# Kernel optimization log

Measured on AMD Instinct MI355X. Metric: run time of the kernel, lower is better.

Reference implementation:

```python
import jax, jax.numpy as jnp
from jax import lax
import numpy as np

DECAY = 0.9
THRESH = 1.0


def setup_inputs() -> dict:
    key = jax.random.key(0)
    k1, k2, k3 = jax.random.split(key, 3)
    B, T, I, H, O = 64, 256, 1024, 2048, 1024
    x = jax.random.normal(k1, (B, T, I), dtype=jnp.float32)
    W1 = jax.random.normal(k2, (I, H), dtype=jnp.float32) * (1.0 / np.sqrt(I))
    b1 = jnp.zeros((H,), dtype=jnp.float32)
    W2 = jax.random.normal(k3, (H, O), dtype=jnp.float32) * (1.0 / np.sqrt(H))
    b2 = jnp.zeros((O,), dtype=jnp.float32)
    return {"x": x, "W1": W1, "b1": b1, "W2": W2, "b2": b2}


def reference(x, W1, b1, W2, b2):
    B, T, I = x.shape
    H = W1.shape[1]
    # Batch fc1 across all timesteps in one GEMM: [B,T,H]
    cur = jnp.einsum('bti,ih->bth', x, W1) + b1
    cur_tm = jnp.swapaxes(cur, 0, 1)  # [T,B,H] time-major for scan

    def step(carry, cur_t):
        mem, _ = carry
        mem = mem * DECAY + cur_t * (1.0 - DECAY)
        fired = mem > THRESH
        spk = jnp.where(fired, 1.0, 0.0).astype(mem.dtype)
        mem = jnp.where(fired, 0.0, mem)
        return (mem, spk), None

    mem0 = jnp.zeros((B, H), dtype=x.dtype)
    spk0 = jnp.zeros((B, H), dtype=x.dtype)
    (_, spk_last), _ = lax.scan(step, (mem0, spk0), cur_tm)
    # fc2 applied only to the final spike pattern, as in the original
    return spk_last @ W2 + b2
```

## Files before the change

### kernel.cpp

```cpp
#include <hip/hip_runtime.h>


typedef __attribute__((ext_vector_type(16))) float f32x16;
typedef __attribute__((ext_vector_type(8))) short s16x8;

#define GPTR(p) ((const __attribute__((address_space(1))) void*)(p))
#define SPTR(p) ((__attribute__((address_space(3))) void*)(p))

static constexpr int Bsz = 64, Tsz = 256, Isz = 1024, Hsz = 2048, Osz = 1024;
static constexpr int BK = 16;
static constexpr int NKT = Isz / BK;
static constexpr int REG = 4096;
static constexpr int AH_OFF = 0, AL_OFF = REG, BH_OFF = 2 * REG, BL_OFF = 3 * REG;
static constexpr int BUFEL = 4 * REG;
static constexpr int ST = 68;
static constexpr int LDS_USHORTS = 3 * BUFEL;

__device__ __forceinline__ unsigned short f2bf(float f) {
  unsigned u = __float_as_uint(f);
  u += 0x7FFFu + ((u >> 16) & 1u);
  return (unsigned short)(u >> 16);
}
__device__ __forceinline__ float bf2f(unsigned short h) {
  return __uint_as_float(((unsigned)h) << 16);
}

__global__ void split_x_kernel(const float* __restrict__ x,
                               unsigned short* __restrict__ hi,
                               unsigned short* __restrict__ lo) {
  const long i = (long)blockIdx.x * 256 + threadIdx.x;
  const float4 v = ((const float4*)x)[i];
  const unsigned short hx = f2bf(v.x), hy = f2bf(v.y), hz = f2bf(v.z), hw = f2bf(v.w);
  ushort4 H, L;
  H.x = hx; H.y = hy; H.z = hz; H.w = hw;
  L.x = f2bf(v.x - bf2f(hx));
  L.y = f2bf(v.y - bf2f(hy));
  L.z = f2bf(v.z - bf2f(hz));
  L.w = f2bf(v.w - bf2f(hw));
  ((ushort4*)hi)[i] = H;
  ((ushort4*)lo)[i] = L;
}

__global__ void w1_transpose_split_kernel(const float* __restrict__ W1,
                                          unsigned short* __restrict__ wh,
                                          unsigned short* __restrict__ wl) {
  __shared__ float tile[32][33];
  const int h0 = blockIdx.x * 32;
  const int i0 = blockIdx.y * 32;
  const int c = threadIdx.x & 31;
  const int r4 = threadIdx.x >> 5;
#pragma unroll
  for (int s = 0; s < 4; ++s) {
    const int r = r4 + s * 8;
    tile[r][c] = W1[(long)(i0 + r) * Hsz + h0 + c];
  }
  __syncthreads();
#pragma unroll
  for (int s = 0; s < 4; ++s) {
    const int hr = r4 + s * 8;
    const float v = tile[c][hr];
    const unsigned short hh = f2bf(v);
    wh[(long)(h0 + hr) * Isz + i0 + c] = hh;
    wl[(long)(h0 + hr) * Isz + i0 + c] = f2bf(v - bf2f(hh));
  }
}

__global__ __launch_bounds__(512, 2) void gemm1_scan_kernel(
    const unsigned short* __restrict__ xh, const unsigned short* __restrict__ xl,
    const unsigned short* __restrict__ wth, const unsigned short* __restrict__ wtl,
    const float* __restrict__ b1, float* __restrict__ spk) {
  __shared__ __align__(16) unsigned short lds[LDS_USHORTS];

  const int tid = threadIdx.x;
  const int l = tid & 63;
  const int w = tid >> 6;
  const int wm = w >> 2;
  const int wn = w & 3;
  const int b = blockIdx.y;
  const int hb = blockIdx.x * 256;

  const int srow = tid >> 1;
  const int gch8 = (tid & 1) * 8;
  const unsigned short* gAh = xh + (long)(b * Tsz + srow) * Isz + gch8;
  const unsigned short* gAl = xl + (long)(b * Tsz + srow) * Isz + gch8;
  const unsigned short* gBh = wth + (long)(hb + srow) * Isz + gch8;
  const unsigned short* gBl = wtl + (long)(hb + srow) * Isz + gch8;

#define STG(OFF, G, Q, KT) do {                                                           \
    unsigned short* d_ = lds + (Q) * BUFEL + (OFF) + tid * 8;                             \
    __builtin_amdgcn_global_load_lds(GPTR((G) + (long)(KT) * BK), SPTR(d_), 16, 0, 0);    \
  } while (0)

  const int lr = l & 31;
  const int abase = (wm * 128 + lr) * BK + (l >> 5) * 8;
  const int bbase = (wn * 64 + lr) * BK + (l >> 5) * 8;

  f32x16 acc[4][2];
#pragma unroll
  for (int i = 0; i < 4; ++i)
#pragma unroll
    for (int j = 0; j < 2; ++j) acc[i][j] = (f32x16)(0.f);

#define MM(MI, NI, AF, BF) \
  acc[MI][NI] = __builtin_amdgcn_mfma_f32_32x32x16_bf16(AF, BF, acc[MI][NI], 0, 0, 0)

#define BAR() __builtin_amdgcn_s_barrier()
#define SBAR() __builtin_amdgcn_sched_barrier(0)
#define WAITLGKM(N) do { asm volatile("s_waitcnt lgkmcnt(" #N ")" ::: "memory"); SBAR(); } while (0)

  STG(AH_OFF, gAh, 0, 0); STG(AL_OFF, gAl, 0, 0);
  STG(BH_OFF, gBh, 0, 0); STG(BL_OFF, gBl, 0, 0);
  STG(AH_OFF, gAh, 1, 1); STG(AL_OFF, gAl, 1, 1);
  STG(BH_OFF, gBh, 1, 1); STG(BL_OFF, gBl, 1, 1);
  asm volatile("s_waitcnt vmcnt(4)" ::: "memory");
  BAR();

  s16x8 Ah[4], Al[4], Bh[2], Bl[2];

  int q = 0;
  for (int kt = 0; kt < NKT; ++kt) {
    const unsigned short* p = lds + q * BUFEL;
    const int qn = (q >= 1) ? q - 1 : 2;
    const bool st = (kt + 2) < NKT;

#pragma unroll
    for (int mi = 0; mi < 4; ++mi) Ah[mi] = *(const s16x8*)(p + AH_OFF + abase + mi * 512);
#pragma unroll
    for (int ni = 0; ni < 2; ++ni) Bh[ni] = *(const s16x8*)(p + BH_OFF + bbase + ni * 512);
    SBAR();
#pragma unroll
    for (int mi = 0; mi < 4; ++mi) Al[mi] = *(const s16x8*)(p + AL_OFF + abase + mi * 512);
#pragma unroll
    for (int ni = 0; ni < 2; ++ni) Bl[ni] = *(const s16x8*)(p + BL_OFF + bbase + ni * 512);
    SBAR();
    if (st) { STG(AH_OFF, gAh, qn, kt + 2); STG(AL_OFF, gAl, qn, kt + 2);
              STG(BH_OFF, gBh, qn, kt + 2); STG(BL_OFF, gBl, qn, kt + 2); }
    SBAR();
    WAITLGKM(6);
    __builtin_amdgcn_s_setprio(1);
#pragma unroll
    for (int mi = 0; mi < 4; ++mi)
#pragma unroll
      for (int ni = 0; ni < 2; ++ni) MM(mi, ni, Ah[mi], Bh[ni]);
    WAITLGKM(0);
#pragma unroll
    for (int mi = 0; mi < 4; ++mi)
#pragma unroll
      for (int ni = 0; ni < 2; ++ni) MM(mi, ni, Ah[mi], Bl[ni]);
#pragma unroll
    for (int mi = 0; mi < 4; ++mi)
#pragma unroll
      for (int ni = 0; ni < 2; ++ni) MM(mi, ni, Al[mi], Bh[ni]);
    __builtin_amdgcn_s_setprio(0);
    if (st) asm volatile("s_waitcnt vmcnt(4)" ::: "memory");
    else    asm volatile("s_waitcnt vmcnt(0)" ::: "memory");
    BAR();
    q = (q == 2) ? 0 : q + 1;
  }

  __syncthreads();
  float* scanbuf = reinterpret_cast<float*>(lds);
  float memv = 0.f;
  int fired = 0;
  const float b1v = (tid < 256) ? b1[hb + tid] : 0.f;

  for (int rnd = 0; rnd < 4; ++rnd) {
    if (wm == (rnd >> 1)) {
      const int mi0 = (rnd & 1) * 2;
#pragma unroll
      for (int dm = 0; dm < 2; ++dm) {
        const int mi = mi0 + dm;
#pragma unroll
        for (int ni = 0; ni < 2; ++ni) {
          const int col = wn * 64 + ni * 32 + lr;
          float* dst = scanbuf + col * ST + dm * 32 + 4 * (l >> 5);
#pragma unroll
          for (int rq = 0; rq < 4; ++rq) {
            float4 v;
            v.x = acc[mi][ni][rq * 4 + 0];
            v.y = acc[mi][ni][rq * 4 + 1];
            v.z = acc[mi][ni][rq * 4 + 2];
            v.w = acc[mi][ni][rq * 4 + 3];
            *reinterpret_cast<float4*>(dst + 8 * rq) = v;
          }
        }
      }
    }
    __syncthreads();
    if (tid < 256) {
      const float* src = scanbuf + tid * ST;
      float4 cur = *reinterpret_cast<const float4*>(src);
      for (int t0 = 0; t0 < 64; t0 += 4) {
        const int tn = (t0 + 4 < 64) ? t0 + 4 : t0;
        const float4 nxt = *reinterpret_cast<const float4*>(src + tn);
        float c;
        c = cur.x + b1v; memv = memv * 0.9f + c * 0.1f; fired = memv > 1.0f; if (fired) memv = 0.f;
        c = cur.y + b1v; memv = memv * 0.9f + c * 0.1f; fired = memv > 1.0f; if (fired) memv = 0.f;
        c = cur.z + b1v; memv = memv * 0.9f + c * 0.1f; fired = memv > 1.0f; if (fired) memv = 0.f;
        c = cur.w + b1v; memv = memv * 0.9f + c * 0.1f; fired = memv > 1.0f; if (fired) memv = 0.f;
        cur = nxt;
      }
    }
    __syncthreads();
  }
  if (tid < 256) spk[(long)b * Hsz + hb + tid] = fired ? 1.0f : 0.0f;
}

__global__ void gemm2_kernel(const float* __restrict__ spk, const float* __restrict__ W2,
                             const float* __restrict__ b2, float* __restrict__ out) {
  __shared__ int s_cnt[256];
  __shared__ int s_off[257];
  __shared__ int s_list[Hsz];
  const int b = blockIdx.x;
  const int tid = threadIdx.x;
  int hs[8];
  int c = 0;
#pragma unroll
  for (int e = 0; e < 8; ++e) {
    const int h = tid * 8 + e;
    if (spk[(long)b * Hsz + h] > 0.5f) hs[c++] = h;
  }
  s_cnt[tid] = c;
  __syncthreads();
  if (tid == 0) {
    int s = 0;
    for (int i = 0; i < 256; ++i) { s_off[i] = s; s += s_cnt[i]; }
    s_off[256] = s;
  }
  __syncthreads();
  {
    const int base = s_off[tid];
    for (int i = 0; i < c; ++i) s_list[base + i] = hs[i];
  }
  __syncthreads();
  const int total = s_off[256];
#pragma unroll
  for (int q = 0; q < 4; ++q) {
    const int o = q * 256 + tid;
    float v = b2[o];
    for (int i = 0; i < total; ++i) v += W2[(long)s_list[i] * Osz + o];
    out[(long)b * Osz + o] = v;
  }
}

extern "C" void kernel_launch(void* const* d_in, const int* in_sizes, int n_in,
                              void* d_out, int out_size, void* d_ws, size_t ws_size,
                              hipStream_t stream) {
  const float* x = (const float*)d_in[0];
  const float* W1 = (const float*)d_in[1];
  const float* b1 = (const float*)d_in[2];
  const float* W2 = (const float*)d_in[3];
  const float* b2 = (const float*)d_in[4];
  float* out = (float*)d_out;

  unsigned short* xh = (unsigned short*)d_ws;
  unsigned short* xl = xh + (long)Bsz * Tsz * Isz;
  unsigned short* wh = xl + (long)Bsz * Tsz * Isz;
  unsigned short* wl = wh + (long)Hsz * Isz;
  float* spk = (float*)(wl + (long)Hsz * Isz);

  split_x_kernel<<<(Bsz * Tsz * Isz) / (256 * 4), 256, 0, stream>>>(x, xh, xl);
  w1_transpose_split_kernel<<<dim3(Hsz / 32, Isz / 32), 256, 0, stream>>>(W1, wh, wl);
  gemm1_scan_kernel<<<dim3(8, 64), 512, 0, stream>>>(xh, xl, wh, wl, b1, spk);
  gemm2_kernel<<<Bsz, 256, 0, stream>>>(spk, W2, b2, out);
}
```

Baseline: 218.6 us.

## Halve GEMM1 H-tile to 128 and raise occupancy to four blocks per CU

Shrinks the per-block H tile from 256 to 128 columns, doubling the grid to 1024 blocks. The warp layout becomes 4x2 with 2x2 MFMA tiles per wave, and launch bounds rise to four blocks per CU. B hi/lo staging is merged into a single load per thread and the hand-scheduled lgkm waits, sched barriers and setprio are removed. The aim is better latency hiding through occupancy and tail balance, at the cost of reloading the x tiles twice as often (lower A reuse) and losing the explicit instruction scheduling.

```diff
diff --git a/kernel.cpp b/kernel.cpp
--- a/kernel.cpp
+++ b/kernel.cpp
@@ -10,9 +10,9 @@
 static constexpr int Bsz = 64, Tsz = 256, Isz = 1024, Hsz = 2048, Osz = 1024;
 static constexpr int BK = 16;
 static constexpr int NKT = Isz / BK;
-static constexpr int REG = 4096;
-static constexpr int AH_OFF = 0, AL_OFF = REG, BH_OFF = 2 * REG, BL_OFF = 3 * REG;
-static constexpr int BUFEL = 4 * REG;
+static constexpr int NB = 128;
+static constexpr int AL_OFF = 4096, B_OFF = 8192;
+static constexpr int BUFEL = 12288;
 static constexpr int ST = 68;
 static constexpr int LDS_USHORTS = 3 * BUFEL;
 
@@ -65,7 +65,7 @@
   }
 }
 
-__global__ __launch_bounds__(512, 2) void gemm1_scan_kernel(
+__global__ __launch_bounds__(512, 4) void gemm1_scan_kernel(
     const unsigned short* __restrict__ xh, const unsigned short* __restrict__ xl,
     const unsigned short* __restrict__ wth, const unsigned short* __restrict__ wtl,
     const float* __restrict__ b1, float* __restrict__ spk) {
@@ -74,106 +74,88 @@
   const int tid = threadIdx.x;
   const int l = tid & 63;
   const int w = tid >> 6;
-  const int wm = w >> 2;
-  const int wn = w & 3;
+  const int wm = w >> 1;
+  const int wn = w & 1;
   const int b = blockIdx.y;
-  const int hb = blockIdx.x * 256;
-
-  const int srow = tid >> 1;
-  const int gch8 = (tid & 1) * 8;
-  const unsigned short* gAh = xh + (long)(b * Tsz + srow) * Isz + gch8;
-  const unsigned short* gAl = xl + (long)(b * Tsz + srow) * Isz + gch8;
-  const unsigned short* gBh = wth + (long)(hb + srow) * Isz + gch8;
-  const unsigned short* gBl = wtl + (long)(hb + srow) * Isz + gch8;
-
-#define STG(OFF, G, Q, KT) do {                                                           \
-    unsigned short* d_ = lds + (Q) * BUFEL + (OFF) + tid * 8;                             \
-    __builtin_amdgcn_global_load_lds(GPTR((G) + (long)(KT) * BK), SPTR(d_), 16, 0, 0);    \
+  const int hb = blockIdx.x * NB;
+
+  const int arow = tid >> 1;
+  const int brow = (tid >> 1) & 127;
+  const int ch8 = (tid & 1) * 8;
+  const unsigned short* gAh = xh + (long)(b * Tsz + arow) * Isz + ch8;
+  const unsigned short* gAl = xl + (long)(b * Tsz + arow) * Isz + ch8;
+  const unsigned short* gB = ((tid < 256) ? wth : wtl) + (long)(hb + brow) * Isz + ch8;
+
+#define STG(Q, KT) do {                                                                   \
+    unsigned short* d_ = lds + (Q) * BUFEL + tid * 8;                                     \
+    __builtin_amdgcn_global_load_lds(GPTR(gAh + (long)(KT) * BK), SPTR(d_), 16, 0, 0);    \
+    __builtin_amdgcn_global_load_lds(GPTR(gAl + (long)(KT) * BK), SPTR(d_ + AL_OFF), 16, 0, 0); \
+    __builtin_amdgcn_global_load_lds(GPTR(gB + (long)(KT) * BK), SPTR(d_ + B_OFF), 16, 0, 0);   \
   } while (0)
 
   const int lr = l & 31;
-  const int abase = (wm * 128 + lr) * BK + (l >> 5) * 8;
-  const int bbase = (wn * 64 + lr) * BK + (l >> 5) * 8;
-
-  f32x16 acc[4][2];
-#pragma unroll
-  for (int i = 0; i < 4; ++i)
+  const int kc = (l >> 5) * 8;
+  const int aoff0 = (wm * 64 + lr) * 16 + kc;
+  const int boff0 = B_OFF + (wn * 64 + lr) * 16 + kc;
+
+  f32x16 acc[2][2];
+#pragma unroll
+  for (int i = 0; i < 2; ++i)
 #pragma unroll
     for (int j = 0; j < 2; ++j) acc[i][j] = (f32x16)(0.f);
 
 #define MM(MI, NI, AF, BF) \
   acc[MI][NI] = __builtin_amdgcn_mfma_f32_32x32x16_bf16(AF, BF, acc[MI][NI], 0, 0, 0)
 
-#define BAR() __builtin_amdgcn_s_barrier()
-#define SBAR() __builtin_amdgcn_sched_barrier(0)
-#define WAITLGKM(N) do { asm volatile("s_waitcnt lgkmcnt(" #N ")" ::: "memory"); SBAR(); } while (0)
-
-  STG(AH_OFF, gAh, 0, 0); STG(AL_OFF, gAl, 0, 0);
-  STG(BH_OFF, gBh, 0, 0); STG(BL_OFF, gBl, 0, 0);
-  STG(AH_OFF, gAh, 1, 1); STG(AL_OFF, gAl, 1, 1);
-  STG(BH_OFF, gBh, 1, 1); STG(BL_OFF, gBl, 1, 1);
-  asm volatile("s_waitcnt vmcnt(4)" ::: "memory");
-  BAR();
-
-  s16x8 Ah[4], Al[4], Bh[2], Bl[2];
-
-  int q = 0;
+  STG(0, 0);
+  STG(1, 1);
+  asm volatile("s_waitcnt vmcnt(3)" ::: "memory");
+  __builtin_amdgcn_s_barrier();
+
   for (int kt = 0; kt < NKT; ++kt) {
+    const int q = kt % 3;
     const unsigned short* p = lds + q * BUFEL;
-    const int qn = (q >= 1) ? q - 1 : 2;
-    const bool st = (kt + 2) < NKT;
-
-#pragma unroll
-    for (int mi = 0; mi < 4; ++mi) Ah[mi] = *(const s16x8*)(p + AH_OFF + abase + mi * 512);
-#pragma unroll
-    for (int ni = 0; ni < 2; ++ni) Bh[ni] = *(const s16x8*)(p + BH_OFF + bbase + ni * 512);
-    SBAR();
-#pragma unroll
-    for (int mi = 0; mi < 4; ++mi) Al[mi] = *(const s16x8*)(p + AL_OFF + abase + mi * 512);
-#pragma unroll
-    for (int ni = 0; ni < 2; ++ni) Bl[ni] = *(const s16x8*)(p + BL_OFF + bbase + ni * 512);
-    SBAR();
-    if (st) { STG(AH_OFF, gAh, qn, kt + 2); STG(AL_OFF, gAl, qn, kt + 2);
-              STG(BH_OFF, gBh, qn, kt + 2); STG(BL_OFF, gBl, qn, kt + 2); }
-    SBAR();
-    WAITLGKM(6);
-    __builtin_amdgcn_s_setprio(1);
-#pragma unroll
-    for (int mi = 0; mi < 4; ++mi)
-#pragma unroll
-      for (int ni = 0; ni < 2; ++ni) MM(mi, ni, Ah[mi], Bh[ni]);
-    WAITLGKM(0);
-#pragma unroll
-    for (int mi = 0; mi < 4; ++mi)
-#pragma unroll
-      for (int ni = 0; ni < 2; ++ni) MM(mi, ni, Ah[mi], Bl[ni]);
-#pragma unroll
-    for (int mi = 0; mi < 4; ++mi)
-#pragma unroll
-      for (int ni = 0; ni < 2; ++ni) MM(mi, ni, Al[mi], Bh[ni]);
-    __builtin_amdgcn_s_setprio(0);
-    if (st) asm volatile("s_waitcnt vmcnt(4)" ::: "memory");
-    else    asm volatile("s_waitcnt vmcnt(0)" ::: "memory");
-    BAR();
-    q = (q == 2) ? 0 : q + 1;
+
+    if (kt + 2 < NKT) {
+      const int qn = (q >= 1) ? q - 1 : 2;
+      STG(qn, kt + 2);
+    }
+
+    s16x8 Ah0 = *(const s16x8*)(p + aoff0);
+    s16x8 Ah1 = *(const s16x8*)(p + aoff0 + 512);
+    s16x8 Al0 = *(const s16x8*)(p + AL_OFF + aoff0);
+    s16x8 Al1 = *(const s16x8*)(p + AL_OFF + aoff0 + 512);
+    s16x8 Bh0 = *(const s16x8*)(p + boff0);
+    s16x8 Bh1 = *(const s16x8*)(p + boff0 + 512);
+    s16x8 Bl0 = *(const s16x8*)(p + boff0 + 2048);
+    s16x8 Bl1 = *(const s16x8*)(p + boff0 + 2048 + 512);
+
+    MM(0, 0, Ah0, Bh0); MM(0, 1, Ah0, Bh1);
+    MM(1, 0, Ah1, Bh0); MM(1, 1, Ah1, Bh1);
+    MM(0, 0, Ah0, Bl0); MM(0, 1, Ah0, Bl1);
+    MM(1, 0, Ah1, Bl0); MM(1, 1, Ah1, Bl1);
+    MM(0, 0, Al0, Bh0); MM(0, 1, Al0, Bh1);
+    MM(1, 0, Al1, Bh0); MM(1, 1, Al1, Bh1);
+
+    if (kt < NKT - 2) asm volatile("s_waitcnt vmcnt(3)" ::: "memory");
+    else              asm volatile("s_waitcnt vmcnt(0)" ::: "memory");
+    __builtin_amdgcn_s_barrier();
   }
 
   __syncthreads();
   float* scanbuf = reinterpret_cast<float*>(lds);
   float memv = 0.f;
   int fired = 0;
-  const float b1v = (tid < 256) ? b1[hb + tid] : 0.f;
+  const float b1v = (tid < NB) ? b1[hb + tid] : 0.f;
 
   for (int rnd = 0; rnd < 4; ++rnd) {
-    if (wm == (rnd >> 1)) {
-      const int mi0 = (rnd & 1) * 2;
-#pragma unroll
-      for (int dm = 0; dm < 2; ++dm) {
-        const int mi = mi0 + dm;
+    if (wm == rnd) {
+#pragma unroll
+      for (int mi = 0; mi < 2; ++mi)
 #pragma unroll
         for (int ni = 0; ni < 2; ++ni) {
           const int col = wn * 64 + ni * 32 + lr;
-          float* dst = scanbuf + col * ST + dm * 32 + 4 * (l >> 5);
+          float* dst = scanbuf + col * ST + mi * 32 + 4 * (l >> 5);
 #pragma unroll
           for (int rq = 0; rq < 4; ++rq) {
             float4 v;
@@ -184,10 +166,9 @@
             *reinterpret_cast<float4*>(dst + 8 * rq) = v;
           }
         }
-      }
     }
     __syncthreads();
-    if (tid < 256) {
+    if (tid < NB) {
       const float* src = scanbuf + tid * ST;
       float4 cur = *reinterpret_cast<const float4*>(src);
       for (int t0 = 0; t0 < 64; t0 += 4) {
@@ -203,7 +184,7 @@
     }
     __syncthreads();
   }
-  if (tid < 256) spk[(long)b * Hsz + hb + tid] = fired ? 1.0f : 0.0f;
+  if (tid < NB) spk[(long)b * Hsz + hb + tid] = fired ? 1.0f : 0.0f;
 }
 
 __global__ void gemm2_kernel(const float* __restrict__ spk, const float* __restrict__ W2,
@@ -261,6 +242,6 @@
 
   split_x_kernel<<<(Bsz * Tsz * Isz) / (256 * 4), 256, 0, stream>>>(x, xh, xl);
   w1_transpose_split_kernel<<<dim3(Hsz / 32, Isz / 32), 256, 0, stream>>>(W1, wh, wl);
-  gemm1_scan_kernel<<<dim3(8, 64), 512, 0, stream>>>(xh, xl, wh, wl, b1, spk);
+  gemm1_scan_kernel<<<dim3(Hsz / NB, Bsz), 512, 0, stream>>>(xh, xl, wh, wl, b1, spk);
   gemm2_kernel<<<Bsz, 256, 0, stream>>>(spk, W2, b2, out);
 }
```

Result: slower. 252.1 us (+15.3%).
